# Kernel optimization log

Measured on AMD Instinct MI355X. Metric: run time of the kernel, lower is better.

## Reference

```python
import jax, jax.numpy as jnp
import numpy as np

N = 100_000      # nodes
D = 64           # in_dim
E = 1_600_000    # edges (avg degree 16)
P_L = 0.5        # leaky slope for low-pass gate
P_H = 0.5        # leaky slope for high-pass gate


def setup_inputs() -> dict:
    key = jax.random.key(0)
    ks = jax.random.split(key, 10)
    h = jax.random.normal(ks[0], (N, D), jnp.float32)
    d = jax.random.uniform(ks[1], (N,), jnp.float32)  # degree norms 1/sqrt(deg)
    src = jax.random.randint(ks[2], (E,), 0, N)
    dst = jax.random.randint(ks[3], (E,), 0, N)
    # xavier_normal(gain=1.414) scale ~ gain*sqrt(2/(fan_in+fan_out))
    sg = 1.414 * np.sqrt(2.0 / (2 * D + 1))
    sr = 1.414 * np.sqrt(2.0 / (2 * D + D))
    Wl = jax.random.normal(ks[4], (1, 2 * D), jnp.float32) * sg
    bl = jnp.zeros((1,), jnp.float32)
    Wh = jax.random.normal(ks[5], (1, 2 * D), jnp.float32) * sg
    bh = jnp.zeros((1,), jnp.float32)
    Wr = jax.random.normal(ks[6], (D, 2 * D), jnp.float32) * sr
    br = jnp.zeros((D,), jnp.float32)
    return {"h": h, "d": d, "src": src, "dst": dst,
            "Wl": Wl, "bl": bl, "Wh": Wh, "bh": bh, "Wr": Wr, "br": br}


def reference(h, d, src, dst, Wl, bl, Wh, bh, Wr, br):
    # gate_x(cat([h_dst, h_src])) == h_dst @ W[:, :D] + h_src @ W[:, D:] + b
    # -> project once per node [N], gather per edge [E] (avoids [E,2D] concat)
    low_dst = h @ Wl[0, :D]
    low_src = h @ Wl[0, D:]
    _low = low_dst[dst] + low_src[src] + bl[0]                     # [E]
    g_low = jnp.tanh(jax.nn.relu(jnp.where(_low > 0, _low, -P_L * _low)))

    high_dst = h @ Wh[0, :D]
    high_src = h @ Wh[0, D:]
    _high = high_dst[dst] + high_src[src] + bh[0]                  # [E]
    g_high = jnp.tanh(-jax.nn.relu(jnp.where(_high > 0, _high, -P_H * _high)))

    dd = d[dst] * d[src]                                           # [E]
    e_low = g_low * dd
    e_high = g_high * dd

    h_src = h[src]                                                 # [E, D]
    z_low = jax.ops.segment_sum(h_src * e_low[:, None], dst, num_segments=N)
    z_high = jax.ops.segment_sum(h_src * e_high[:, None], dst, num_segments=N)

    z = jnp.concatenate([z_low, z_high], axis=1)                   # [N, 2D]
    return z @ Wr.T + br                                           # [N, D]
```

## Files before the change

### kernel.cpp

```cpp
#include <hip/hip_runtime.h>
#include <hip/hip_fp16.h>
#include <math.h>

#define N_NODES 100000
#define D_DIM   64
#define N_EDGES 1600000
#define P_L 0.5f
#define P_H 0.5f

#define NPB   32
#define NB    3125
#define TILE  2048
#define NT    784
#define GRP   28
#define GT    28
#define CAP   768
#define ZS    132


typedef unsigned int uint;
typedef unsigned short ushort_t;

__device__ inline ushort_t f2bf(float f) {
    uint u = __float_as_uint(f);
    uint r = (u + 0x7fffu + ((u >> 16) & 1u)) >> 16;
    return (ushort_t)r;
}

__device__ inline float tanh_pos(float x) {
    return 1.f - 2.f / (__expf(2.f * x) + 1.f);
}

__device__ inline void fma16(uint gy, uint4 hv, float* acc) {
    float el = __half2float(__ushort_as_half((unsigned short)(gy & 0xffffu)));
    float eh = __half2float(__ushort_as_half((unsigned short)(gy >> 16)));
    float f0 = __uint_as_float(hv.x << 16);
    float f1 = __uint_as_float(hv.x & 0xffff0000u);
    float f2 = __uint_as_float(hv.y << 16);
    float f3 = __uint_as_float(hv.y & 0xffff0000u);
    float f4 = __uint_as_float(hv.z << 16);
    float f5 = __uint_as_float(hv.z & 0xffff0000u);
    float f6 = __uint_as_float(hv.w << 16);
    float f7 = __uint_as_float(hv.w & 0xffff0000u);
    acc[0]  += el * f0; acc[1]  += el * f1; acc[2]  += el * f2; acc[3]  += el * f3;
    acc[4]  += el * f4; acc[5]  += el * f5; acc[6]  += el * f6; acc[7]  += el * f7;
    acc[8]  += eh * f0; acc[9]  += eh * f1; acc[10] += eh * f2; acc[11] += eh * f3;
    acc[12] += eh * f4; acc[13] += eh * f5; acc[14] += eh * f6; acc[15] += eh * f7;
}

__global__ __launch_bounds__(256) void node_gates_kernel(
    const float* __restrict__ h, const float* __restrict__ dvec,
    const float* __restrict__ Wl, const float* __restrict__ Wh,
    ushort_t* __restrict__ hbf,
    float4* __restrict__ gdst4, float4* __restrict__ gsrc4)
{
    int tid = threadIdx.x;
    int lane = tid & 63;
    int half = lane >> 5;
    int l32 = lane & 31;
    int node = blockIdx.x * 8 + (tid >> 6) * 2 + half;

    float2 hv2 = *(const float2*)(h + (size_t)node * 64 + l32 * 2);
    uint pk = (uint)f2bf(hv2.x) | ((uint)f2bf(hv2.y) << 16);
    ((uint*)hbf)[(size_t)node * 32 + l32] = pk;

    float pld = hv2.x * Wl[2 * l32]      + hv2.y * Wl[2 * l32 + 1];
    float pls = hv2.x * Wl[64 + 2 * l32] + hv2.y * Wl[64 + 2 * l32 + 1];
    float phd = hv2.x * Wh[2 * l32]      + hv2.y * Wh[2 * l32 + 1];
    float phs = hv2.x * Wh[64 + 2 * l32] + hv2.y * Wh[64 + 2 * l32 + 1];
    #pragma unroll
    for (int m = 16; m >= 1; m >>= 1) {
        pld += __shfl_xor(pld, m);
        pls += __shfl_xor(pls, m);
        phd += __shfl_xor(phd, m);
        phs += __shfl_xor(phs, m);
    }
    if (l32 == 0) {
        float d = dvec[node];
        gdst4[node] = make_float4(pld, phd, d, 0.f);
        gsrc4[node] = make_float4(pls, phs, d, 0.f);
    }
}

__global__ __launch_bounds__(512) void bucket_hist_kernel(const int* __restrict__ dst,
                                                          int* __restrict__ T) {
    __shared__ int hist[NB];
    int tid = threadIdx.x;
    for (int i = tid; i < NB; i += 512) hist[i] = 0;
    __syncthreads();
    int base = blockIdx.x * TILE;
    #pragma unroll
    for (int j = 0; j < TILE / 512; ++j) {
        int e = base + j * 512 + tid;
        if (e < N_EDGES) atomicAdd(&hist[dst[e] >> 5], 1);
    }
    __syncthreads();
    int* row = T + (size_t)blockIdx.x * NB;
    for (int i = tid; i < NB; i += 512) row[i] = hist[i];
}

__global__ __launch_bounds__(1024) void scanA1_kernel(int* __restrict__ T,
                                                      int* __restrict__ S) {
    int b = blockIdx.x * 1024 + threadIdx.x;
    if (b >= NB) return;
    int g = blockIdx.y;
    int run = 0;
    #pragma unroll
    for (int w = g * GT; w < g * GT + GT; ++w) {
        int idx = w * NB + b;
        int v = T[idx];
        T[idx] = run;
        run += v;
    }
    S[(size_t)g * NB + b] = run;
}

__global__ __launch_bounds__(1024) void scanA2_kernel(int* __restrict__ S,
                                                      int* __restrict__ totG) {
    int b = blockIdx.x * 1024 + threadIdx.x;
    if (b >= NB) return;
    int run = 0;
    #pragma unroll
    for (int g = 0; g < GRP; ++g) {
        int idx = g * NB + b;
        int v = S[idx];
        S[idx] = run;
        run += v;
    }
    totG[b] = run;
}

__global__ __launch_bounds__(1024) void scanB_kernel(const int* __restrict__ totG,
                                                     int* __restrict__ baseG,
                                                     int* __restrict__ bucketoffs,
                                                     const float* __restrict__ Wr,
                                                     float* __restrict__ wrt) {
    int tid = threadIdx.x;
    for (int idx = tid; idx < 64 * 128; idx += 1024) {
        int c = idx >> 7;
        int k = idx & 127;
        wrt[k * 64 + c] = Wr[idx];
    }

    __shared__ int scan_lds[1024];
    int a[4];
    int s = 0;
    #pragma unroll
    for (int i = 0; i < 4; ++i) {
        int b = tid * 4 + i;
        a[i] = (b < NB) ? totG[b] : 0;
        s += a[i];
    }
    scan_lds[tid] = s;
    __syncthreads();
    for (int d = 1; d < 1024; d <<= 1) {
        int v = (tid >= d) ? scan_lds[tid - d] : 0;
        __syncthreads();
        scan_lds[tid] += v;
        __syncthreads();
    }
    int excl = scan_lds[tid] - s;
    int total = scan_lds[1023];
    #pragma unroll
    for (int i = 0; i < 4; ++i) {
        int b = tid * 4 + i;
        if (b < NB) { baseG[b] = excl; bucketoffs[b] = excl; }
        excl += a[i];
    }
    if (tid == 0) bucketoffs[NB] = total;
}

__global__ __launch_bounds__(512) void place_kernel(
    const int* __restrict__ src, const int* __restrict__ dst,
    const int* __restrict__ T, const int* __restrict__ S,
    const int* __restrict__ baseG,
    const float4* __restrict__ gdst4, const float4* __restrict__ gsrc4,
    const float* __restrict__ bl, const float* __restrict__ bh,
    uint2* __restrict__ ebuf)
{
    __shared__ int cur[NB];
    int tid = threadIdx.x;
    const int* row  = T + (size_t)blockIdx.x * NB;
    const int* Srow = S + (size_t)(blockIdx.x / GT) * NB;
    for (int i = tid; i < NB; i += 512) cur[i] = row[i] + Srow[i] + baseG[i];
    __syncthreads();

    float bl0 = bl[0], bh0 = bh[0];
    int base = blockIdx.x * TILE;
    #pragma unroll
    for (int j = 0; j < TILE / 512; ++j) {
        int e = base + j * 512 + tid;
        if (e >= N_EDGES) continue;
        int t = dst[e];
        int s = src[e];
        float4 gt = gdst4[t];
        float4 gs = gsrc4[s];
        float xl = gt.x + gs.x + bl0;
        float xh = gt.y + gs.y + bh0;
        float ll = xl > 0.f ? xl : -P_L * xl;
        float hh = xh > 0.f ? xh : -P_H * xh;
        float dd = gt.z * gs.z;
        float el =  tanh_pos(ll) * dd;
        float eh = -tanh_pos(hh) * dd;
        uint ge = (uint)__half_as_ushort(__float2half_rn(el))
                | ((uint)__half_as_ushort(__float2half_rn(eh)) << 16);
        int b  = t >> 5;
        uint dl = (uint)(t & 31);
        int pos = atomicAdd(&cur[b], 1);
        ebuf[pos] = make_uint2((uint)s | (dl << 17), ge);
    }
}

__global__ __launch_bounds__(512) void accum_final_kernel(
    const int* __restrict__ bucketoffs, const uint2* __restrict__ ebuf,
    const ushort_t* __restrict__ hbf, const float* __restrict__ wrt,
    const float* __restrict__ br, float* __restrict__ out)
{
    __shared__ float z[NPB * ZS];
    __shared__ uint2 srec[CAP];
    __shared__ int ncount[NPB];
    __shared__ int nbase[NPB];
    __shared__ int ncur[NPB];

    int tid = threadIdx.x;
    int bk = blockIdx.x;
    int beg = bucketoffs[bk];
    int end = bucketoffs[bk + 1];
    int cnt = end - beg;
    if (cnt > CAP) cnt = CAP;

    if (tid < NPB) ncount[tid] = 0;

    bool hA = tid < cnt;
    bool hB = tid + 512 < cnt;
    uint2 rA = hA ? ebuf[beg + tid] : make_uint2(0, 0);
    uint2 rB = hB ? ebuf[beg + tid + 512] : make_uint2(0, 0);
    __syncthreads();

    if (hA) atomicAdd(&ncount[(rA.x >> 17) & 31], 1);
    if (hB) atomicAdd(&ncount[(rB.x >> 17) & 31], 1);
    __syncthreads();

    if (tid < 32) {
        int v = ncount[tid];
        int p = v;
        #pragma unroll
        for (int d = 1; d < 32; d <<= 1) {
            int x = __shfl_up(p, d);
            if (tid >= d) p += x;
        }
        nbase[tid] = p - v;
        ncur[tid]  = p - v;
    }
    __syncthreads();

    if (hA) {
        int dl = (rA.x >> 17) & 31;
        srec[atomicAdd(&ncur[dl], 1)] = rA;
    }
    if (hB) {
        int dl = (rB.x >> 17) & 31;
        srec[atomicAdd(&ncur[dl], 1)] = rB;
    }
    __syncthreads();

    int sg = tid >> 3;
    int l8 = tid & 7;
    int node4 = sg >> 1;
    int par = sg & 1;
    int rbeg = nbase[node4];
    int rend = ncur[node4];

    float acc[16];
    #pragma unroll
    for (int j = 0; j < 16; ++j) acc[j] = 0.f;

    int k = rbeg + par;
    for (; k + 6 < rend; k += 8) {
        uint2 r0 = srec[k];
        uint2 r1 = srec[k + 2];
        uint2 r2 = srec[k + 4];
        uint2 r3 = srec[k + 6];
        uint4 h0 = *(const uint4*)(hbf + (size_t)(r0.x & 0x1FFFF) * 64 + l8 * 8);
        uint4 h1 = *(const uint4*)(hbf + (size_t)(r1.x & 0x1FFFF) * 64 + l8 * 8);
        uint4 h2 = *(const uint4*)(hbf + (size_t)(r2.x & 0x1FFFF) * 64 + l8 * 8);
        uint4 h3 = *(const uint4*)(hbf + (size_t)(r3.x & 0x1FFFF) * 64 + l8 * 8);
        fma16(r0.y, h0, acc);
        fma16(r1.y, h1, acc);
        fma16(r2.y, h2, acc);
        fma16(r3.y, h3, acc);
    }
    for (; k < rend; k += 2) {
        uint2 r0 = srec[k];
        uint4 hv = *(const uint4*)(hbf + (size_t)(r0.x & 0x1FFFF) * 64 + l8 * 8);
        fma16(r0.y, hv, acc);
    }

    float* zp = &z[node4 * ZS + l8 * 8];
    if (par == 0) {
        *(float4*)(zp + 0)  = make_float4(acc[0],  acc[1],  acc[2],  acc[3]);
        *(float4*)(zp + 4)  = make_float4(acc[4],  acc[5],  acc[6],  acc[7]);
        *(float4*)(zp + 64) = make_float4(acc[8],  acc[9],  acc[10], acc[11]);
        *(float4*)(zp + 68) = make_float4(acc[12], acc[13], acc[14], acc[15]);
    }
    __syncthreads();
    if (par == 1) {
        float4 z0 = *(float4*)(zp + 0);
        float4 z1 = *(float4*)(zp + 4);
        float4 z2 = *(float4*)(zp + 64);
        float4 z3 = *(float4*)(zp + 68);
        *(float4*)(zp + 0)  = make_float4(z0.x + acc[0],  z0.y + acc[1],  z0.z + acc[2],  z0.w + acc[3]);
        *(float4*)(zp + 4)  = make_float4(z1.x + acc[4],  z1.y + acc[5],  z1.z + acc[6],  z1.w + acc[7]);
        *(float4*)(zp + 64) = make_float4(z2.x + acc[8],  z2.y + acc[9],  z2.z + acc[10], z2.w + acc[11]);
        *(float4*)(zp + 68) = make_float4(z3.x + acc[12], z3.y + acc[13], z3.z + acc[14], z3.w + acc[15]);
    }
    __syncthreads();

    int node = tid >> 4;
    int g = tid & 15;
    float facc[4] = {0.f, 0.f, 0.f, 0.f};
    const float* zrow = z + node * ZS;
    #pragma unroll 2
    for (int kk = 0; kk < 128; kk += 4) {
        float4 z4 = *(const float4*)(zrow + kk);
        const float* wp = wrt + kk * 64 + g * 4;
        float4 w0 = *(const float4*)(wp);
        float4 w1 = *(const float4*)(wp + 64);
        float4 w2 = *(const float4*)(wp + 128);
        float4 w3 = *(const float4*)(wp + 192);
        facc[0] += z4.x * w0.x + z4.y * w1.x + z4.z * w2.x + z4.w * w3.x;
        facc[1] += z4.x * w0.y + z4.y * w1.y + z4.z * w2.y + z4.w * w3.y;
        facc[2] += z4.x * w0.z + z4.y * w1.z + z4.z * w2.z + z4.w * w3.z;
        facc[3] += z4.x * w0.w + z4.y * w1.w + z4.z * w2.w + z4.w * w3.w;
    }
    int n = bk * NPB + node;
    float* op = out + (size_t)n * 64 + g * 4;
    const float* bp = br + g * 4;
    *(float4*)(op) = make_float4(facc[0] + bp[0], facc[1] + bp[1], facc[2] + bp[2], facc[3] + bp[3]);
}

extern "C" void kernel_launch(void* const* d_in, const int* in_sizes, int n_in,
                              void* d_out, int out_size, void* d_ws, size_t ws_size,
                              hipStream_t stream) {
    const float* h    = (const float*)d_in[0];
    const float* dvec = (const float*)d_in[1];
    const int*   src  = (const int*)  d_in[2];
    const int*   dst  = (const int*)  d_in[3];
    const float* Wl   = (const float*)d_in[4];
    const float* bl   = (const float*)d_in[5];
    const float* Wh   = (const float*)d_in[6];
    const float* bh   = (const float*)d_in[7];
    const float* Wr   = (const float*)d_in[8];
    const float* br   = (const float*)d_in[9];
    float* out = (float*)d_out;

    char* ws = (char*)d_ws;
    size_t off = 0;
    auto alloc = [&](size_t bytes) { char* p = ws + off; off += (bytes + 255) & ~size_t(255); return p; };

    ushort_t* hbf       = (ushort_t*)alloc((size_t)N_NODES * 64 * 2);
    float4*   gdst4     = (float4*)  alloc((size_t)N_NODES * 16);
    float4*   gsrc4     = (float4*)  alloc((size_t)N_NODES * 16);
    float*    wrt       = (float*)   alloc(64 * 128 * 4);
    int*      T         = (int*)     alloc((size_t)NT * NB * 4);
    int*      S         = (int*)     alloc((size_t)GRP * NB * 4);
    int*      totG      = (int*)     alloc((size_t)NB * 4);
    int*      baseG     = (int*)     alloc((size_t)NB * 4);
    int*      bucketoffs= (int*)     alloc((size_t)(NB + 1) * 4);
    uint2*    ebuf      = (uint2*)   alloc((size_t)N_EDGES * 8);

    node_gates_kernel<<<N_NODES / 8, 256, 0, stream>>>(h, dvec, Wl, Wh, hbf, gdst4, gsrc4);
    bucket_hist_kernel<<<NT, 512, 0, stream>>>(dst, T);
    {
        dim3 g1((NB + 1023) / 1024, GRP);
        scanA1_kernel<<<g1, 1024, 0, stream>>>(T, S);
    }
    scanA2_kernel<<<(NB + 1023) / 1024, 1024, 0, stream>>>(S, totG);
    scanB_kernel<<<1, 1024, 0, stream>>>(totG, baseG, bucketoffs, Wr, wrt);
    place_kernel<<<NT, 512, 0, stream>>>(src, dst, T, S, baseG, gdst4, gsrc4, bl, bh, ebuf);
    accum_final_kernel<<<NB, 512, 0, stream>>>(bucketoffs, ebuf, hbf, wrt, br, out);
}
```

Baseline: 296.8 us.

## Packed f2 FMAs, warp-aggregated bucket atomics, and early hbf row prefetch

Rewrites the accumulation and final projection with 2-wide float vectors so the compiler can emit packed FMA instructions. Replaces per-thread LDS atomics in the counting sort with ballot-based matching, so one leader per wavefront does the atomic and the others get their rank by popcount. It also touches the source hbf rows right after loading the edge records, before the barrier, to warm the cache for the later gather. The costs are extra ballot and shuffle work, and the prefetch loads, which may be wasted if the lines are evicted before use.

```diff
diff --git a/kernel.cpp b/kernel.cpp
--- a/kernel.cpp
+++ b/kernel.cpp
@@ -20,6 +20,7 @@
 
 typedef unsigned int uint;
 typedef unsigned short ushort_t;
+typedef float f2 __attribute__((ext_vector_type(2)));
 
 __device__ inline ushort_t f2bf(float f) {
     uint u = __float_as_uint(f);
@@ -31,21 +32,25 @@
     return 1.f - 2.f / (__expf(2.f * x) + 1.f);
 }
 
-__device__ inline void fma16(uint gy, uint4 hv, float* acc) {
+__device__ inline void fma16(uint gy, uint4 hv, f2* acc) {
     float el = __half2float(__ushort_as_half((unsigned short)(gy & 0xffffu)));
     float eh = __half2float(__ushort_as_half((unsigned short)(gy >> 16)));
-    float f0 = __uint_as_float(hv.x << 16);
-    float f1 = __uint_as_float(hv.x & 0xffff0000u);
-    float f2 = __uint_as_float(hv.y << 16);
-    float f3 = __uint_as_float(hv.y & 0xffff0000u);
-    float f4 = __uint_as_float(hv.z << 16);
-    float f5 = __uint_as_float(hv.z & 0xffff0000u);
-    float f6 = __uint_as_float(hv.w << 16);
-    float f7 = __uint_as_float(hv.w & 0xffff0000u);
-    acc[0]  += el * f0; acc[1]  += el * f1; acc[2]  += el * f2; acc[3]  += el * f3;
-    acc[4]  += el * f4; acc[5]  += el * f5; acc[6]  += el * f6; acc[7]  += el * f7;
-    acc[8]  += eh * f0; acc[9]  += eh * f1; acc[10] += eh * f2; acc[11] += eh * f3;
-    acc[12] += eh * f4; acc[13] += eh * f5; acc[14] += eh * f6; acc[15] += eh * f7;
+    f2 f01 = {__uint_as_float(hv.x << 16), __uint_as_float(hv.x & 0xffff0000u)};
+    f2 f23 = {__uint_as_float(hv.y << 16), __uint_as_float(hv.y & 0xffff0000u)};
+    f2 f45 = {__uint_as_float(hv.z << 16), __uint_as_float(hv.z & 0xffff0000u)};
+    f2 f67 = {__uint_as_float(hv.w << 16), __uint_as_float(hv.w & 0xffff0000u)};
+    acc[0] += f01 * el; acc[1] += f23 * el; acc[2] += f45 * el; acc[3] += f67 * el;
+    acc[4] += f01 * eh; acc[5] += f23 * eh; acc[6] += f45 * eh; acc[7] += f67 * eh;
+}
+
+__device__ inline unsigned long long match_dl(int dl, bool active) {
+    unsigned long long m = __ballot(active);
+    #pragma unroll
+    for (int b = 0; b < 5; ++b) {
+        unsigned long long bal = __ballot(active && ((dl >> b) & 1));
+        m &= ((dl >> b) & 1) ? bal : ~bal;
+    }
+    return m;
 }
 
 __global__ __launch_bounds__(256) void node_gates_kernel(
@@ -223,6 +228,7 @@
     __shared__ int ncur[NPB];
 
     int tid = threadIdx.x;
+    int lane = tid & 63;
     int bk = blockIdx.x;
     int beg = bucketoffs[bk];
     int end = bucketoffs[bk + 1];
@@ -235,10 +241,27 @@
     bool hB = tid + 512 < cnt;
     uint2 rA = hA ? ebuf[beg + tid] : make_uint2(0, 0);
     uint2 rB = hB ? ebuf[beg + tid + 512] : make_uint2(0, 0);
-    __syncthreads();
-
-    if (hA) atomicAdd(&ncount[(rA.x >> 17) & 31], 1);
-    if (hB) atomicAdd(&ncount[(rB.x >> 17) & 31], 1);
+
+    {
+        const uint* pa = (const uint*)(hbf + (size_t)(rA.x & 0x1FFFF) * 64);
+        const uint* pb = (const uint*)(hbf + (size_t)(rB.x & 0x1FFFF) * 64);
+        uint p0 = hA ? pa[0]  : 0u;
+        uint p1 = hA ? pa[16] : 0u;
+        uint p2 = hB ? pb[0]  : 0u;
+        uint p3 = hB ? pb[16] : 0u;
+        asm volatile("" :: "v"(p0), "v"(p1), "v"(p2), "v"(p3));
+    }
+    __syncthreads();
+
+    int dlA = (int)((rA.x >> 17) & 31u);
+    int dlB = (int)((rB.x >> 17) & 31u);
+
+    unsigned long long mA = match_dl(dlA, hA);
+    if (hA && lane == (int)__builtin_ctzll(mA))
+        atomicAdd(&ncount[dlA], (int)__popcll(mA));
+    unsigned long long mB = match_dl(dlB, hB);
+    if (hB && lane == (int)__builtin_ctzll(mB))
+        atomicAdd(&ncount[dlB], (int)__popcll(mB));
     __syncthreads();
 
     if (tid < 32) {
@@ -255,12 +278,20 @@
     __syncthreads();
 
     if (hA) {
-        int dl = (rA.x >> 17) & 31;
-        srec[atomicAdd(&ncur[dl], 1)] = rA;
+        int ldr = (int)__builtin_ctzll(mA);
+        int base = 0;
+        if (lane == ldr) base = atomicAdd(&ncur[dlA], (int)__popcll(mA));
+        base = __shfl(base, ldr);
+        int rank = (int)__popcll(mA & ((1ull << lane) - 1ull));
+        srec[base + rank] = rA;
     }
     if (hB) {
-        int dl = (rB.x >> 17) & 31;
-        srec[atomicAdd(&ncur[dl], 1)] = rB;
+        int ldr = (int)__builtin_ctzll(mB);
+        int base = 0;
+        if (lane == ldr) base = atomicAdd(&ncur[dlB], (int)__popcll(mB));
+        base = __shfl(base, ldr);
+        int rank = (int)__popcll(mB & ((1ull << lane) - 1ull));
+        srec[base + rank] = rB;
     }
     __syncthreads();
 
@@ -271,9 +302,9 @@
     int rbeg = nbase[node4];
     int rend = ncur[node4];
 
-    float acc[16];
-    #pragma unroll
-    for (int j = 0; j < 16; ++j) acc[j] = 0.f;
+    f2 acc[8];
+    #pragma unroll
+    for (int j = 0; j < 8; ++j) acc[j] = (f2){0.f, 0.f};
 
     int k = rbeg + par;
     for (; k + 6 < rend; k += 8) {
@@ -298,10 +329,10 @@
 
     float* zp = &z[node4 * ZS + l8 * 8];
     if (par == 0) {
-        *(float4*)(zp + 0)  = make_float4(acc[0],  acc[1],  acc[2],  acc[3]);
-        *(float4*)(zp + 4)  = make_float4(acc[4],  acc[5],  acc[6],  acc[7]);
-        *(float4*)(zp + 64) = make_float4(acc[8],  acc[9],  acc[10], acc[11]);
-        *(float4*)(zp + 68) = make_float4(acc[12], acc[13], acc[14], acc[15]);
+        *(float4*)(zp + 0)  = make_float4(acc[0].x, acc[0].y, acc[1].x, acc[1].y);
+        *(float4*)(zp + 4)  = make_float4(acc[2].x, acc[2].y, acc[3].x, acc[3].y);
+        *(float4*)(zp + 64) = make_float4(acc[4].x, acc[4].y, acc[5].x, acc[5].y);
+        *(float4*)(zp + 68) = make_float4(acc[6].x, acc[6].y, acc[7].x, acc[7].y);
     }
     __syncthreads();
     if (par == 1) {
@@ -309,16 +340,16 @@
         float4 z1 = *(float4*)(zp + 4);
         float4 z2 = *(float4*)(zp + 64);
         float4 z3 = *(float4*)(zp + 68);
-        *(float4*)(zp + 0)  = make_float4(z0.x + acc[0],  z0.y + acc[1],  z0.z + acc[2],  z0.w + acc[3]);
-        *(float4*)(zp + 4)  = make_float4(z1.x + acc[4],  z1.y + acc[5],  z1.z + acc[6],  z1.w + acc[7]);
-        *(float4*)(zp + 64) = make_float4(z2.x + acc[8],  z2.y + acc[9],  z2.z + acc[10], z2.w + acc[11]);
-        *(float4*)(zp + 68) = make_float4(z3.x + acc[12], z3.y + acc[13], z3.z + acc[14], z3.w + acc[15]);
+        *(float4*)(zp + 0)  = make_float4(z0.x + acc[0].x, z0.y + acc[0].y, z0.z + acc[1].x, z0.w + acc[1].y);
+        *(float4*)(zp + 4)  = make_float4(z1.x + acc[2].x, z1.y + acc[2].y, z1.z + acc[3].x, z1.w + acc[3].y);
+        *(float4*)(zp + 64) = make_float4(z2.x + acc[4].x, z2.y + acc[4].y, z2.z + acc[5].x, z2.w + acc[5].y);
+        *(float4*)(zp + 68) = make_float4(z3.x + acc[6].x, z3.y + acc[6].y, z3.z + acc[7].x, z3.w + acc[7].y);
     }
     __syncthreads();
 
     int node = tid >> 4;
     int g = tid & 15;
-    float facc[4] = {0.f, 0.f, 0.f, 0.f};
+    f2 fa0 = {0.f, 0.f}, fa1 = {0.f, 0.f};
     const float* zrow = z + node * ZS;
     #pragma unroll 2
     for (int kk = 0; kk < 128; kk += 4) {
@@ -328,15 +359,15 @@
         float4 w1 = *(const float4*)(wp + 64);
         float4 w2 = *(const float4*)(wp + 128);
         float4 w3 = *(const float4*)(wp + 192);
-        facc[0] += z4.x * w0.x + z4.y * w1.x + z4.z * w2.x + z4.w * w3.x;
-        facc[1] += z4.x * w0.y + z4.y * w1.y + z4.z * w2.y + z4.w * w3.y;
-        facc[2] += z4.x * w0.z + z4.y * w1.z + z4.z * w2.z + z4.w * w3.z;
-        facc[3] += z4.x * w0.w + z4.y * w1.w + z4.z * w2.w + z4.w * w3.w;
+        fa0 += (f2){w0.x, w0.y} * z4.x; fa1 += (f2){w0.z, w0.w} * z4.x;
+        fa0 += (f2){w1.x, w1.y} * z4.y; fa1 += (f2){w1.z, w1.w} * z4.y;
+        fa0 += (f2){w2.x, w2.y} * z4.z; fa1 += (f2){w2.z, w2.w} * z4.z;
+        fa0 += (f2){w3.x, w3.y} * z4.w; fa1 += (f2){w3.z, w3.w} * z4.w;
     }
     int n = bk * NPB + node;
     float* op = out + (size_t)n * 64 + g * 4;
     const float* bp = br + g * 4;
-    *(float4*)(op) = make_float4(facc[0] + bp[0], facc[1] + bp[1], facc[2] + bp[2], facc[3] + bp[3]);
+    *(float4*)(op) = make_float4(fa0.x + bp[0], fa0.y + bp[1], fa1.x + bp[2], fa1.y + bp[3]);
 }
 
 extern "C" void kernel_launch(void* const* d_in, const int* in_sizes, int n_in,
```

Result: slower. 305.9 us (+3.1%).
